# Kernel tuning notes

Measured on AMD Instinct MI355X. Metric: run time of the kernel, lower is better.

The kernel has to match this reference:

```python
import jax, jax.numpy as jnp
import numpy as np

EMBED_DIM = 1024
NUM_HEADS = 16
HEAD_DIM = EMBED_DIM // NUM_HEADS
SCALE = HEAD_DIM ** -0.5


def setup_inputs() -> dict:
    key = jax.random.key(0)
    k1, k2, k3, k4, k5, k6 = jax.random.split(key, 6)
    B, Tq, Tk = 2, 2048, 2048
    std = EMBED_DIM ** -0.5
    return {
        "x_q": jax.random.normal(k1, (B, Tq, EMBED_DIM), jnp.float32),
        "x_kv": jax.random.normal(k2, (B, Tk, EMBED_DIM), jnp.float32),
        "w_q": jax.random.normal(k3, (EMBED_DIM, EMBED_DIM), jnp.float32) * std,
        "w_kv": jax.random.normal(k4, (EMBED_DIM, 2 * EMBED_DIM), jnp.float32) * std,
        "w_proj": jax.random.normal(k5, (EMBED_DIM, EMBED_DIM), jnp.float32) * std,
        "w_rel": jax.random.normal(k6, (1, NUM_HEADS), jnp.float32) * 0.02,
    }


def reference(x_q, x_kv, w_q, w_kv, w_proj, w_rel):
    B, Tq, _ = x_q.shape
    Tk = x_kv.shape[1]
    # projections
    q = x_q @ w_q                       # [B,Tq,E]
    kv = x_kv @ w_kv                    # [B,Tk,2E]
    k, v = jnp.split(kv, 2, axis=-1)

    def heads(y, T):
        return y.reshape(B, T, NUM_HEADS, HEAD_DIM).transpose(0, 2, 1, 3)

    q = heads(q, Tq)                    # [B,H,Tq,D]
    k = heads(k, Tk)
    v = heads(v, Tk)

    logits = jnp.einsum('bhqd,bhkd->bhqk', q, k) * SCALE  # [B,H,Tq,Tk]

    # relative position bias: Dense(1 -> H) applied to (pos_q - pos_k)
    rel = jnp.arange(Tq, dtype=jnp.float32)[:, None] - jnp.arange(Tk, dtype=jnp.float32)[None, :]
    bias = rel[..., None] * w_rel[0]                      # [Tq,Tk,H]
    bias = bias.transpose(2, 0, 1)[None]                  # [1,H,Tq,Tk]
    logits = logits + bias

    attn = jax.nn.softmax(logits, axis=-1)                # dropout=0 / inference -> identity
    out = jnp.einsum('bhqk,bhkd->bhqd', attn, v)          # [B,H,Tq,D]
    out = out.transpose(0, 2, 1, 3).reshape(B, Tq, EMBED_DIM)
    return out @ w_proj
```

## Files before the change

kernel.cpp:

```cpp
#include <hip/hip_runtime.h>
#include <hip/hip_bf16.h>

typedef __attribute__((ext_vector_type(8))) short short8;
typedef __attribute__((ext_vector_type(8))) __bf16 bf16x8;
typedef __attribute__((ext_vector_type(4))) float f32x4;
typedef __attribute__((ext_vector_type(8))) unsigned short ushort8v;
typedef __attribute__((ext_vector_type(4))) unsigned short ushort4v;

#define NB 2
#define TQ 2048
#define TKK 2048
#define EMB 1024
#define NH 16
#define HD 64

__device__ __forceinline__ unsigned short f2bf(float f){
  union { float f; unsigned u; } v; v.f = f;
  unsigned r = v.u + 0x7FFFu + ((v.u >> 16) & 1u);
  return (unsigned short)(r >> 16);
}

#define GLOAD_LDS16(g, l) __builtin_amdgcn_global_load_lds( \
    (const __attribute__((address_space(1))) void*)(g), \
    (__attribute__((address_space(3))) void*)(l), 16, 0, 0)

#define SWZ(row, inner) ((inner) ^ (((row)&7)<<4))

__device__ __forceinline__ void mfma16(const short8& a, const short8& b, f32x4& c){
  c = __builtin_amdgcn_mfma_f32_16x16x32_bf16(
        __builtin_bit_cast(bf16x8, a), __builtin_bit_cast(bf16x8, b), c, 0, 0, 0);
}

__global__ __launch_bounds__(256) void cvt_f32_bf16(const float* __restrict__ in,
    unsigned short* __restrict__ out, int n4){
  int i = blockIdx.x*256 + threadIdx.x;
  if (i >= n4) return;
  float4 v = ((const float4*)in)[i];
  ushort4v o;
  o.x = f2bf(v.x); o.y = f2bf(v.y); o.z = f2bf(v.z); o.w = f2bf(v.w);
  ((ushort4v*)out)[i] = o;
}

__global__ __launch_bounds__(256) void wt_transpose(const float* __restrict__ W,
    unsigned short* __restrict__ WT, int K, int N){
  __shared__ unsigned short tile[64][72];
  int k0 = blockIdx.y*64, n0 = blockIdx.x*64;
  int tid = threadIdx.x;
  #pragma unroll
  for (int it=0; it<4; ++it){
    int c = tid + it*256;
    int r = c>>4, c4 = (c&15)*4;
    float4 v = *(const float4*)(W + (long)(k0+r)*N + n0 + c4);
    tile[r][c4+0]=f2bf(v.x); tile[r][c4+1]=f2bf(v.y);
    tile[r][c4+2]=f2bf(v.z); tile[r][c4+3]=f2bf(v.w);
  }
  __syncthreads();
  #pragma unroll
  for (int it=0; it<2; ++it){
    int c = tid + it*256;
    int n = c>>3, k8 = (c&7)*8;
    ushort8v o;
    #pragma unroll
    for (int j=0;j<8;++j) o[j] = tile[k8+j][n];
    *(ushort8v*)(WT + (long)(n0+n)*K + k0 + k8) = o;
  }
}

__global__ __launch_bounds__(256) void v_transpose(const unsigned short* __restrict__ KV,
    unsigned short* __restrict__ VT){
  __shared__ unsigned short tile[64][72];
  int bh = blockIdx.y; int b = bh>>4, h = bh&15;
  int t0 = blockIdx.x*64;
  int tid = threadIdx.x;
  #pragma unroll
  for (int it=0; it<2; ++it){
    int c = tid + it*256;
    int r = c>>3, d8 = (c&7)*8;
    ushort8v v = *(const ushort8v*)(KV + (long)(b*TKK + t0 + r)*(2*EMB) + EMB + h*HD + d8);
    #pragma unroll
    for (int j=0;j<8;++j) tile[r][d8+j] = v[j];
  }
  __syncthreads();
  #pragma unroll
  for (int it=0; it<2; ++it){
    int c = tid + it*256;
    int d = c>>3, t8 = (c&7)*8;
    ushort8v o;
    #pragma unroll
    for (int j=0;j<8;++j) o[j] = tile[t8+j][d];
    *(ushort8v*)(VT + (long)(bh*HD + d)*TKK + t0 + t8) = o;
  }
}

template<int OUT_BF16>
__device__ __forceinline__ void gemm_body(const unsigned short* __restrict__ A,
    const unsigned short* __restrict__ BT, void* __restrict__ Cout,
    int M, int N, int K, int m0, int n0,
    unsigned short* Al, unsigned short* Bl){
  const int tid = threadIdx.x;
  const int wave = tid>>6, lane = tid&63;
  const int wm = (wave>>1)*64, wn = (wave&1)*64;
  const int g = lane>>4, lr = lane&15;
  const int srow = lane>>3;
  const int sinner = (lane&7)*16;
  f32x4 acc[4][4] = {};

  for (int k0=0; k0<K; k0+=64){
    #pragma unroll
    for (int j=0;j<4;++j){
      int chunk = wave*4 + j;
      int row = chunk*8 + srow;
      int kb = SWZ(row, sinner);
      GLOAD_LDS16(A + (long)(m0+row)*K + k0 + (kb>>1), Al + chunk*512);
      GLOAD_LDS16(BT + (long)(n0+row)*K + k0 + (kb>>1), Bl + chunk*512);
    }
    __syncthreads();
    #pragma unroll
    for (int kk=0;kk<2;++kk){
      short8 af[4], bfr[4];
      const int kbyte = kk*64 + g*16;
      #pragma unroll
      for (int i=0;i<4;++i){
        int ar = wm + i*16 + lr;
        af[i] = *(const short8*)((const char*)Al + ar*128 + SWZ(ar, kbyte));
        int br = wn + i*16 + lr;
        bfr[i] = *(const short8*)((const char*)Bl + br*128 + SWZ(br, kbyte));
      }
      #pragma unroll
      for (int i=0;i<4;++i)
        #pragma unroll
        for (int jn=0;jn<4;++jn)
          mfma16(af[i], bfr[jn], acc[i][jn]);
    }
    __syncthreads();
  }
  #pragma unroll
  for (int i=0;i<4;++i){
    int row = m0 + wm + i*16 + g*4;
    #pragma unroll
    for (int jn=0;jn<4;++jn){
      int col = n0 + wn + jn*16 + lr;
      #pragma unroll
      for (int r=0;r<4;++r){
        if (OUT_BF16)
          ((unsigned short*)Cout)[(long)(row+r)*N + col] = f2bf(acc[i][jn][r]);
        else
          ((float*)Cout)[(long)(row+r)*N + col] = acc[i][jn][r];
      }
    }
  }
}

template<int OUT_BF16>
__global__ __launch_bounds__(256,3) void gemm_bt(const unsigned short* __restrict__ A,
    const unsigned short* __restrict__ BT, void* __restrict__ Cout,
    int M, int N, int K){
  __shared__ unsigned short Al[128*64];
  __shared__ unsigned short Bl[128*64];
  gemm_body<OUT_BF16>(A, BT, Cout, M, N, K, blockIdx.y*128, blockIdx.x*128, Al, Bl);
}

__global__ __launch_bounds__(256,3) void gemm_qkv(
    const unsigned short* __restrict__ Aq,  const unsigned short* __restrict__ WqT,  unsigned short* __restrict__ Qb,
    const unsigned short* __restrict__ Akv, const unsigned short* __restrict__ WkvT, unsigned short* __restrict__ KVb){
  __shared__ unsigned short Al[128*64];
  __shared__ unsigned short Bl[128*64];
  const int x = blockIdx.x;
  if (x < 8)
    gemm_body<1>(Aq,  WqT,  Qb,  NB*TQ, EMB,   EMB, blockIdx.y*128, x*128,     Al, Bl);
  else
    gemm_body<1>(Akv, WkvT, KVb, NB*TKK, 2*EMB, EMB, blockIdx.y*128, (x-8)*128, Al, Bl);
}

#define PPITCH 144
__global__ __launch_bounds__(512,4) void attn_kernel(const unsigned short* __restrict__ Qb,
    const unsigned short* __restrict__ KVb, const unsigned short* __restrict__ VT,
    const float* __restrict__ w_rel, unsigned short* __restrict__ Ob){
  __shared__ unsigned short Kl[64*64];
  __shared__ unsigned short Vl[64*64];
  __shared__ __attribute__((aligned(16))) char Pl[8][16*PPITCH];
  const int id  = blockIdx.x + 16*blockIdx.y;
  const int nid = (id & 7)*64 + (id >> 3);
  const int qb  = nid & 15, bh = nid >> 4;
  const int b = bh>>4, h = bh&15;
  const int q0 = qb*128;
  const int tid = threadIdx.x, wave = tid>>6, lane = tid&63;
  const int g = lane>>4, lr = lane&15;
  const int srow = lane>>3, sinner = (lane&7)*16;
  const float C1 = 0.125f*1.44269504f;
  const float wr2 = w_rel[h]*1.44269504f;
  const float w64 = 64.0f*wr2;
  char* Pw = &Pl[wave][0];

  short8 qf[2];
  #pragma unroll
  for (int kk=0;kk<2;++kk)
    qf[kk] = *(const short8*)(Qb + (long)(b*TQ + q0 + wave*16 + lr)*EMB + h*HD + kk*32 + g*8);

  const float bq = (float)(q0 + wave*16 + lr)*wr2;
  float dl[4][4];
  #pragma unroll
  for (int n=0;n<4;++n)
    #pragma unroll
    for (int r=0;r<4;++r)
      dl[n][r] = bq - (float)(n*16 + 4*g + r)*wr2;

  short8 ones;
  #pragma unroll
  for (int j=0;j<8;++j) ones[j] = (short)0x3F80;

  f32x4 oacc[4] = {};
  f32x4 lacc = {};
  float Mx = -1e30f;

  for (int kt=0; kt<TKK; kt+=64){
    {
      int row = wave*8 + srow;
      int kb = SWZ(row, sinner);
      GLOAD_LDS16(KVb + (long)(b*TKK + kt + row)*(2*EMB) + h*HD + (kb>>1), Kl + wave*512);
      GLOAD_LDS16(VT + (long)(bh*HD + row)*TKK + kt + (kb>>1), Vl + wave*512);
    }
    __syncthreads();

    f32x4 sacc[4] = {};
    #pragma unroll
    for (int kk=0;kk<2;++kk){
      short8 kf[4];
      const int kbyte = kk*64 + g*16;
      #pragma unroll
      for (int n=0;n<4;++n){
        int trow = n*16 + lr;
        kf[n] = *(const short8*)((const char*)Kl + trow*128 + SWZ(trow, kbyte));
      }
      #pragma unroll
      for (int n=0;n<4;++n)
        mfma16(kf[n], qf[kk], sacc[n]);
    }

    #pragma unroll
    for (int n=0;n<4;++n)
      #pragma unroll
      for (int r=0;r<4;++r)
        sacc[n][r] = fmaf(sacc[n][r], C1, dl[n][r]);

    float rowmax;
    {
      float x0 = fmaxf(fmaxf(sacc[0][0],sacc[0][1]), fmaxf(sacc[0][2],sacc[0][3]));
      float x1 = fmaxf(fmaxf(sacc[1][0],sacc[1][1]), fmaxf(sacc[1][2],sacc[1][3]));
      float x2 = fmaxf(fmaxf(sacc[2][0],sacc[2][1]), fmaxf(sacc[2][2],sacc[2][3]));
      float x3 = fmaxf(fmaxf(sacc[3][0],sacc[3][1]), fmaxf(sacc[3][2],sacc[3][3]));
      rowmax = fmaxf(fmaxf(x0,x1), fmaxf(x2,x3));
      rowmax = fmaxf(rowmax, __shfl_xor(rowmax, 16, 64));
      rowmax = fmaxf(rowmax, __shfl_xor(rowmax, 32, 64));
    }

    if (__any(rowmax > Mx + 8.0f)){
      float Mn = fmaxf(Mx, rowmax);
      float rf = exp2f(Mx - Mn);
      Mx = Mn;
      float rfo[4];
      #pragma unroll
      for (int r=0;r<4;++r) rfo[r] = __shfl(rf, 4*g + r, 64);
      #pragma unroll
      for (int n=0;n<4;++n)
        #pragma unroll
        for (int r=0;r<4;++r) oacc[n][r] *= rfo[r];
      #pragma unroll
      for (int r=0;r<4;++r) lacc[r] *= rfo[r];
    }

    #pragma unroll
    for (int n=0;n<4;++n){
      ushort4v w;
      #pragma unroll
      for (int r=0;r<4;++r)
        w[r] = __builtin_bit_cast(unsigned short, __float2bfloat16(exp2f(sacc[n][r]-Mx)));
      *(ushort4v*)(Pw + lr*PPITCH + SWZ(lr, 32*n + 8*g)) = w;
    }

    asm volatile("" ::: "memory");

    #pragma unroll
    for (int kk=0;kk<2;++kk){
      const int kbyte = kk*64 + g*16;
      short8 pf = *(const short8*)(Pw + lr*PPITCH + SWZ(lr, kbyte));
      #pragma unroll
      for (int n=0;n<4;++n){
        int vrow = n*16 + lr;
        short8 vf = *(const short8*)((const char*)Vl + vrow*128 + SWZ(vrow, kbyte));
        mfma16(pf, vf, oacc[n]);
      }
      mfma16(pf, ones, lacc);
    }

    #pragma unroll
    for (int n=0;n<4;++n)
      #pragma unroll
      for (int r=0;r<4;++r)
        dl[n][r] -= w64;

    __syncthreads();
  }

  #pragma unroll
  for (int r=0;r<4;++r){
    float inv = 1.0f / lacc[r];
    int q = q0 + wave*16 + 4*g + r;
    #pragma unroll
    for (int n=0;n<4;++n){
      int d = n*16 + lr;
      Ob[(long)(b*TQ + q)*EMB + h*HD + d] = f2bf(oacc[n][r]*inv);
    }
  }
}

extern "C" void kernel_launch(void* const* d_in, const int* in_sizes, int n_in,
                              void* d_out, int out_size, void* d_ws, size_t ws_size,
                              hipStream_t stream){
  const float* x_q    = (const float*)d_in[0];
  const float* x_kv   = (const float*)d_in[1];
  const float* w_q    = (const float*)d_in[2];
  const float* w_kv   = (const float*)d_in[3];
  const float* w_proj = (const float*)d_in[4];
  const float* w_rel  = (const float*)d_in[5];
  (void)in_sizes; (void)n_in; (void)out_size; (void)ws_size;
  char* ws = (char*)d_ws;
  const size_t MB = 1024*1024;
  unsigned short* Qb   = (unsigned short*)(ws + 0);
  unsigned short* KVb  = (unsigned short*)(ws + 8*MB);
  unsigned short* WpT  = (unsigned short*)(ws + 24*MB);
  unsigned short* WqT  = (unsigned short*)(ws + 26*MB);
  unsigned short* WkvT = (unsigned short*)(ws + 28*MB);
  unsigned short* Aq   = (unsigned short*)(ws + 32*MB);
  unsigned short* Akv  = (unsigned short*)(ws + 40*MB);
  unsigned short* Ob   = Aq;
  unsigned short* VTt  = Akv;
  float* out = (float*)d_out;

  cvt_f32_bf16<<<4096, 256, 0, stream>>>(x_q,  Aq,  (NB*TQ*EMB)/4);
  cvt_f32_bf16<<<4096, 256, 0, stream>>>(x_kv, Akv, (NB*TKK*EMB)/4);
  wt_transpose<<<dim3(16,16), 256, 0, stream>>>(w_q,    WqT,  EMB, EMB);
  wt_transpose<<<dim3(32,16), 256, 0, stream>>>(w_kv,   WkvT, EMB, 2*EMB);
  wt_transpose<<<dim3(16,16), 256, 0, stream>>>(w_proj, WpT,  EMB, EMB);
  gemm_qkv<<<dim3(24,32), 256, 0, stream>>>(Aq, WqT, Qb, Akv, WkvT, KVb);
  v_transpose<<<dim3(32,32), 256, 0, stream>>>(KVb, VTt);
  attn_kernel<<<dim3(16,32), 512, 0, stream>>>(Qb, KVb, VTt, w_rel, Ob);
  gemm_bt<0><<<dim3(8,32),  256, 0, stream>>>(Ob, WpT, out, NB*TQ, EMB, EMB);
}
```

Before: 174.5 us.

## Double-buffer K/V tiles in attention and shrink P scratch pitch

The attention loop now keeps two LDS buffers for K and V. It issues the async global-to-LDS load for the next 64-key tile before computing on the current one, and drops the per-iteration pre-compute barrier. The goal is to hide global load latency behind the QK and PV MFMAs. To offset the larger LDS footprint, the per-wave P scratch pitch drops from 144 to 128 bytes and relies on the swizzle alone to avoid bank conflicts. LDS per block still rises noticeably, which may cut the number of resident blocks per CU below the launch-bounds target.

```diff
diff --git a/kernel.cpp b/kernel.cpp
--- a/kernel.cpp
+++ b/kernel.cpp
@@ -172,13 +172,12 @@
     gemm_body<1>(Akv, WkvT, KVb, NB*TKK, 2*EMB, EMB, blockIdx.y*128, (x-8)*128, Al, Bl);
 }
 
-#define PPITCH 144
 __global__ __launch_bounds__(512,4) void attn_kernel(const unsigned short* __restrict__ Qb,
     const unsigned short* __restrict__ KVb, const unsigned short* __restrict__ VT,
     const float* __restrict__ w_rel, unsigned short* __restrict__ Ob){
-  __shared__ unsigned short Kl[64*64];
-  __shared__ unsigned short Vl[64*64];
-  __shared__ __attribute__((aligned(16))) char Pl[8][16*PPITCH];
+  __shared__ unsigned short Kl[2][64*64];
+  __shared__ unsigned short Vl[2][64*64];
+  __shared__ __attribute__((aligned(16))) char Pl[8][16*128];
   const int id  = blockIdx.x + 16*blockIdx.y;
   const int nid = (id & 7)*64 + (id >> 3);
   const int qb  = nid & 15, bh = nid >> 4;
@@ -192,6 +191,11 @@
   const float w64 = 64.0f*wr2;
   char* Pw = &Pl[wave][0];
 
+  const int strow = wave*8 + srow;
+  const int skb = SWZ(strow, sinner);
+  const unsigned short* Kg = KVb + (long)(b*TKK + strow)*(2*EMB) + h*HD + (skb>>1);
+  const unsigned short* Vg = VT + (long)(bh*HD + strow)*TKK + (skb>>1);
+
   short8 qf[2];
   #pragma unroll
   for (int kk=0;kk<2;++kk)
@@ -213,14 +217,16 @@
   f32x4 lacc = {};
   float Mx = -1e30f;
 
+  GLOAD_LDS16(Kg, &Kl[0][wave*512]);
+  GLOAD_LDS16(Vg, &Vl[0][wave*512]);
+  __syncthreads();
+
+  int cur = 0;
   for (int kt=0; kt<TKK; kt+=64){
-    {
-      int row = wave*8 + srow;
-      int kb = SWZ(row, sinner);
-      GLOAD_LDS16(KVb + (long)(b*TKK + kt + row)*(2*EMB) + h*HD + (kb>>1), Kl + wave*512);
-      GLOAD_LDS16(VT + (long)(bh*HD + row)*TKK + kt + (kb>>1), Vl + wave*512);
-    }
-    __syncthreads();
+    if (kt + 64 < TKK){
+      GLOAD_LDS16(Kg + (long)(kt+64)*(2*EMB), &Kl[cur^1][wave*512]);
+      GLOAD_LDS16(Vg + (kt+64), &Vl[cur^1][wave*512]);
+    }
 
     f32x4 sacc[4] = {};
     #pragma unroll
@@ -230,7 +236,7 @@
       #pragma unroll
       for (int n=0;n<4;++n){
         int trow = n*16 + lr;
-        kf[n] = *(const short8*)((const char*)Kl + trow*128 + SWZ(trow, kbyte));
+        kf[n] = *(const short8*)((const char*)&Kl[cur][0] + trow*128 + SWZ(trow, kbyte));
       }
       #pragma unroll
       for (int n=0;n<4;++n)
@@ -275,7 +281,7 @@
       #pragma unroll
       for (int r=0;r<4;++r)
         w[r] = __builtin_bit_cast(unsigned short, __float2bfloat16(exp2f(sacc[n][r]-Mx)));
-      *(ushort4v*)(Pw + lr*PPITCH + SWZ(lr, 32*n + 8*g)) = w;
+      *(ushort4v*)(Pw + lr*128 + SWZ(lr, 32*n + 8*g)) = w;
     }
 
     asm volatile("" ::: "memory");
@@ -283,11 +289,11 @@
     #pragma unroll
     for (int kk=0;kk<2;++kk){
       const int kbyte = kk*64 + g*16;
-      short8 pf = *(const short8*)(Pw + lr*PPITCH + SWZ(lr, kbyte));
+      short8 pf = *(const short8*)(Pw + lr*128 + SWZ(lr, kbyte));
       #pragma unroll
       for (int n=0;n<4;++n){
         int vrow = n*16 + lr;
-        short8 vf = *(const short8*)((const char*)Vl + vrow*128 + SWZ(vrow, kbyte));
+        short8 vf = *(const short8*)((const char*)&Vl[cur][0] + vrow*128 + SWZ(vrow, kbyte));
         mfma16(pf, vf, oacc[n]);
       }
       mfma16(pf, ones, lacc);
@@ -300,6 +306,7 @@
         dl[n][r] -= w64;
 
     __syncthreads();
+    cur ^= 1;
   }
 
   #pragma unroll
```

Measured after the change: 163.4 us. 6.4% less time.
